# Kernel optimization log

Measured on AMD Instinct MI355X. Metric: run time of the kernel, lower is better.

## Reference

```python
import jax, jax.numpy as jnp
import numpy as np

DIM = 192
HEADS = 6
HSP = 8
WSP = 8
POS_DIM = (DIM // 4) // 4  # 12


def _ln(x, g, b, eps=1e-5):
    m = jnp.mean(x, -1, keepdims=True)
    v = jnp.mean((x - m) ** 2, -1, keepdims=True)
    return (x - m) / jnp.sqrt(v + eps) * g + b


def _rel_tables():
    # rpe_biases: ((2*HSP-1)*(2*WSP-1), 2) float coords of all relative offsets
    bh, bw = np.meshgrid(np.arange(1 - HSP, HSP), np.arange(1 - WSP, WSP), indexing='ij')
    biases = np.stack([bh, bw], -1).reshape(-1, 2).astype(np.float32)
    # relative_position_index: (N, N) int lookup into the bias table
    ch, cw = np.meshgrid(np.arange(HSP), np.arange(WSP), indexing='ij')
    coords = np.stack([ch, cw], 0).reshape(2, -1)  # (2, N)
    rel = coords[:, :, None] - coords[:, None, :]  # (2, N, N)
    idx = (rel[0] + HSP - 1) * (2 * WSP - 1) + (rel[1] + WSP - 1)
    return jnp.asarray(biases), jnp.asarray(idx.astype(np.int32))


def setup_inputs() -> dict:
    key = jax.random.key(0)
    ks = jax.random.split(key, 8)
    B, H, W = 2, 256, 256
    L = H * W
    def lin(k, i, o):
        return jax.random.normal(k, (i, o), jnp.float32) * 0.02
    return {
        'qkv': jax.random.normal(ks[0], (3, B, L, DIM), jnp.float32),
        'w_proj': lin(ks[1], 2, POS_DIM), 'b_proj': jnp.zeros((POS_DIM,), jnp.float32),
        'g1': jnp.ones((POS_DIM,), jnp.float32), 'be1': jnp.zeros((POS_DIM,), jnp.float32),
        'w1': lin(ks[2], POS_DIM, POS_DIM), 'b1': jnp.zeros((POS_DIM,), jnp.float32),
        'g2': jnp.ones((POS_DIM,), jnp.float32), 'be2': jnp.zeros((POS_DIM,), jnp.float32),
        'w2': lin(ks[3], POS_DIM, POS_DIM), 'b2': jnp.zeros((POS_DIM,), jnp.float32),
        'g3': jnp.ones((POS_DIM,), jnp.float32), 'be3': jnp.zeros((POS_DIM,), jnp.float32),
        'w3': lin(ks[4], POS_DIM, HEADS), 'b3': jnp.zeros((HEADS,), jnp.float32),
        'H': H, 'W': W,
    }


def reference(qkv, w_proj, b_proj, g1, be1, w1, b1, g2, be2, w2, b2, g3, be3, w3, b3, H, W):
    B, L, C = qkv.shape[1], qkv.shape[2], qkv.shape[3]
    hd = C // HEADS
    scale = float(hd) ** -0.5
    N = HSP * WSP

    def im2win(x):
        # (B, L, C) -> (B*nW, heads, N, hd)
        x = x.reshape(B, H // HSP, HSP, W // WSP, WSP, C)
        x = x.transpose(0, 1, 3, 2, 4, 5).reshape(-1, N, HEADS, hd)
        return x.transpose(0, 2, 1, 3)

    q = im2win(qkv[0]) * scale
    k = im2win(qkv[1])
    v = im2win(qkv[2])

    attn = jnp.einsum('whnd,whmd->whnm', q, k)  # (B*nW, heads, N, N)

    # dynamic relative position bias via MLP (DynamicPosBias, residual=False)
    biases, rel_idx = _rel_tables()
    p = biases @ w_proj + b_proj
    p = jax.nn.relu(_ln(p, g1, be1)) @ w1 + b1
    p = jax.nn.relu(_ln(p, g2, be2)) @ w2 + b2
    p = jax.nn.relu(_ln(p, g3, be3)) @ w3 + b3  # (n_rel, heads)
    rpb = p[rel_idx.reshape(-1)].reshape(N, N, HEADS).transpose(2, 0, 1)  # (heads, N, N)
    attn = attn + rpb[None]

    attn = jax.nn.softmax(attn, axis=-1)
    x = jnp.einsum('whnm,whmd->whnd', attn, v)  # (B*nW, heads, N, hd)
    x = x.transpose(0, 2, 1, 3).reshape(-1, N, C)

    # windows2img: (B*nW, N, C) -> (B, H, W, C)
    x = x.reshape(B, H // HSP, W // WSP, HSP, WSP, C)
    x = x.transpose(0, 1, 3, 2, 4, 5).reshape(B, H, W, C)
    return x
```

## Files before the change

### kernel.cpp

```cpp
#include <hip/hip_runtime.h>
#include <hip/hip_bf16.h>

#define NHEADS 6
#define HD 32
#define CDIM 192
#define NTOK 64
#define NREL 225
#define PDIM 12
#define IMG 256
#define NWIN 2048
#define SCALE 0.17677669529663687f
#define INV_SCALE 5.656854249492381f

typedef __attribute__((ext_vector_type(8))) short v8s;
typedef __attribute__((ext_vector_type(4))) float v4f;

#define KS2 200
#define VTS 72
#define PTS 72

__device__ __forceinline__ unsigned pkbf(float x, float y) {
    __hip_bfloat162 h = __float22bfloat162_rn(make_float2(x, y));
    union { __hip_bfloat162 h; unsigned u; } c; c.h = h;
    return c.u;
}

__device__ __forceinline__ void ln_relu12(const float* x, const float* g,
                                          const float* be, float* y) {
    float m = 0.f;
#pragma unroll
    for (int i = 0; i < PDIM; ++i) m += x[i];
    m *= (1.f / PDIM);
    float v = 0.f;
#pragma unroll
    for (int i = 0; i < PDIM; ++i) { float d = x[i] - m; v += d * d; }
    v *= (1.f / PDIM);
    float inv = rsqrtf(v + 1e-5f);
#pragma unroll
    for (int i = 0; i < PDIM; ++i) {
        float t = (x[i] - m) * inv * g[i] + be[i];
        y[i] = t > 0.f ? t : 0.f;
    }
}

__global__ __launch_bounds__(256) void win_attn_fused(
    const float* __restrict__ qkv,
    const float* __restrict__ wp, const float* __restrict__ bp,
    const float* __restrict__ g1, const float* __restrict__ be1,
    const float* __restrict__ w1, const float* __restrict__ b1,
    const float* __restrict__ g2, const float* __restrict__ be2,
    const float* __restrict__ w2, const float* __restrict__ b2,
    const float* __restrict__ g3, const float* __restrict__ be3,
    const float* __restrict__ w3, const float* __restrict__ b3,
    float* __restrict__ out)
{
    __shared__ __align__(16) unsigned short ks[NTOK * KS2];
    __shared__ __align__(16) unsigned short vt[CDIM * VTS];
    __shared__ __align__(16) unsigned short pt[NTOK * PTS];
    __shared__ float psh[NHEADS * NREL];

    const int t = threadIdx.x;
    const int win = blockIdx.x;
    const int b  = win >> 10;
    const int bh = (win >> 5) & 31;
    const int bw = win & 31;

    const int lane = t & 63;
    const int wave = t >> 6;
    const int lw = lane & 15;
    const int lg = lane >> 4;
    const int rowbase = wave * 16;

    const size_t PL = (size_t)2 * IMG * IMG * CDIM;
    const float* qplane = qkv + (size_t)b * IMG * IMG * CDIM;
    const float* kplane = qplane + PL;
    const float* vplane = kplane + PL;

    auto pixoff = [&](int tok) -> size_t {
        return ((size_t)(bh * 8 + (tok >> 3)) * IMG + (bw * 8 + (tok & 7))) * CDIM;
    };

#pragma unroll
    for (int pass = 0; pass < 12; ++pass) {
        int fidx = t + pass * 256;
        int s   = fidx / 384;
        int rem = fidx - s * 384;
        int j1  = rem / 48;
        int f   = rem - j1 * 48;
        float4 k4 = *(const float4*)(kplane
                     + ((size_t)(bh * 8 + s) * IMG + (bw * 8 + j1)) * CDIM + f * 4);
        uint2 kk; kk.x = pkbf(k4.x, k4.y); kk.y = pkbf(k4.z, k4.w);
        *(uint2*)&ks[(s * 8 + j1) * KS2 + f * 4] = kk;
    }

    {
        const int u  = t & 31;
        const int dg = t >> 5;
        const int ta = (u & 15) + (u >> 4) * 32;
        const int db = dg * 4;
        const int kpa = (u & 15) * 4 + (u >> 4) * 2;
        const size_t offa = pixoff(ta), offb = pixoff(ta + 16);
#pragma unroll
        for (int h = 0; h < NHEADS; ++h) {
            float4 va = *(const float4*)(vplane + offa + h * HD + db);
            float4 vb = *(const float4*)(vplane + offb + h * HD + db);
            int row = h * HD + db;
            *(unsigned*)&vt[(row + 0) * VTS + kpa] = pkbf(va.x, vb.x);
            *(unsigned*)&vt[(row + 1) * VTS + kpa] = pkbf(va.y, vb.y);
            *(unsigned*)&vt[(row + 2) * VTS + kpa] = pkbf(va.z, vb.z);
            *(unsigned*)&vt[(row + 3) * VTS + kpa] = pkbf(va.w, vb.w);
        }
    }

    v8s aq[NHEADS];
    {
        const size_t qoff = pixoff(rowbase + lw);
#pragma unroll
        for (int h = 0; h < NHEADS; ++h) {
            const float* qp = qplane + qoff + h * HD + lg * 8;
            float4 q0 = *(const float4*)qp;
            float4 q1 = *(const float4*)(qp + 4);
            union { v8s v; unsigned x[4]; } au;
            au.x[0] = pkbf(q0.x, q0.y);
            au.x[1] = pkbf(q0.z, q0.w);
            au.x[2] = pkbf(q1.x, q1.y);
            au.x[3] = pkbf(q1.z, q1.w);
            aq[h] = au.v;
        }
    }

    if (t < NREL) {
        float x0 = (float)(t / 15 - 7);
        float x1 = (float)(t % 15 - 7);
        float h[PDIM], y[PDIM];
#pragma unroll
        for (int o = 0; o < PDIM; ++o)
            h[o] = x0 * wp[o] + x1 * wp[PDIM + o] + bp[o];
        ln_relu12(h, g1, be1, y);
#pragma unroll
        for (int o = 0; o < PDIM; ++o) {
            float a = b1[o];
#pragma unroll
            for (int i = 0; i < PDIM; ++i) a += y[i] * w1[i * PDIM + o];
            h[o] = a;
        }
        ln_relu12(h, g2, be2, y);
#pragma unroll
        for (int o = 0; o < PDIM; ++o) {
            float a = b2[o];
#pragma unroll
            for (int i = 0; i < PDIM; ++i) a += y[i] * w2[i * PDIM + o];
            h[o] = a;
        }
        ln_relu12(h, g3, be3, y);
#pragma unroll
        for (int o = 0; o < NHEADS; ++o) {
            float a = b3[o];
#pragma unroll
            for (int i = 0; i < PDIM; ++i) a += y[i] * w3[i * NHEADS + o];
            psh[o * NREL + t] = a * INV_SCALE;
        }
    }
    __syncthreads();

    int base_r[4];
    size_t ooff[4];
#pragma unroll
    for (int r = 0; r < 4; ++r) {
        int n = rowbase + lg * 4 + r;
        base_r[r] = ((n >> 3) - (lw >> 3) + 7) * 15 + (n & 7) - (lw & 7) + 7;
        ooff[r] = ((size_t)(b * IMG + bh * 8 + (n >> 3)) * IMG
                   + (bw * 8 + (n & 7))) * CDIM;
    }

#pragma unroll
    for (int h = 0; h < NHEADS; ++h) {
        v4f acc[4];
#pragma unroll
        for (int ct = 0; ct < 4; ++ct) {
            v4f z = {0.f, 0.f, 0.f, 0.f};
            v8s bfr = *(const v8s*)&ks[(ct * 16 + lw) * KS2 + h * HD + lg * 8];
            acc[ct] = __builtin_amdgcn_mfma_f32_16x16x32_bf16(aq[h], bfr, z, 0, 0, 0);
        }
        const float* ph = &psh[h * NREL];
        v4f s4 = {0.f, 0.f, 0.f, 0.f};
#pragma unroll
        for (int ct = 0; ct < 4; ++ct)
#pragma unroll
            for (int r = 0; r < 4; ++r) {
                float e = __expf((acc[ct][r] + ph[base_r[r] - ct * 30]) * SCALE);
                acc[ct][r] = e;
                s4[r] += e;
            }
#pragma unroll
        for (int off = 1; off < 16; off <<= 1)
#pragma unroll
            for (int r = 0; r < 4; ++r)
                s4[r] += __shfl_xor(s4[r], off);
        v4f rinv;
#pragma unroll
        for (int r = 0; r < 4; ++r) rinv[r] = __builtin_amdgcn_rcpf(s4[r]);
#pragma unroll
        for (int r = 0; r < 4; ++r) {
            uint2 w;
            w.x = pkbf(acc[0][r], acc[1][r]);
            w.y = pkbf(acc[2][r], acc[3][r]);
            *(uint2*)&pt[(rowbase + lg * 4 + r) * PTS + lw * 4] = w;
        }
        v8s pa[2];
#pragma unroll
        for (int kt = 0; kt < 2; ++kt)
            pa[kt] = *(const v8s*)&pt[(rowbase + lw) * PTS + kt * 32 + lg * 8];
        v4f acc2[2] = {};
#pragma unroll
        for (int dt = 0; dt < 2; ++dt)
#pragma unroll
            for (int kt = 0; kt < 2; ++kt) {
                v8s vb = *(const v8s*)&vt[(h * HD + dt * 16 + lw) * VTS
                                          + kt * 32 + lg * 8];
                acc2[dt] = __builtin_amdgcn_mfma_f32_16x16x32_bf16(pa[kt], vb, acc2[dt], 0, 0, 0);
            }
#pragma unroll
        for (int dt = 0; dt < 2; ++dt)
#pragma unroll
            for (int r = 0; r < 4; ++r)
                out[ooff[r] + h * HD + dt * 16 + lw] = acc2[dt][r] * rinv[r];
    }
}

extern "C" void kernel_launch(void* const* d_in, const int* in_sizes, int n_in,
                              void* d_out, int out_size, void* d_ws, size_t ws_size,
                              hipStream_t stream) {
    const float* qkv = (const float*)d_in[0];
    win_attn_fused<<<NWIN, 256, 0, stream>>>(
        qkv,
        (const float*)d_in[1], (const float*)d_in[2],
        (const float*)d_in[3], (const float*)d_in[4],
        (const float*)d_in[5], (const float*)d_in[6],
        (const float*)d_in[7], (const float*)d_in[8],
        (const float*)d_in[9], (const float*)d_in[10],
        (const float*)d_in[11], (const float*)d_in[12],
        (const float*)d_in[13], (const float*)d_in[14],
        (float*)d_out);
}
```

Before: 92.45 us.

## Split heads across two wave groups with 512-thread blocks per window

Doubles the block to 512 threads, with waves 0-3 handling heads 0-2 and waves 4-7 handling heads 3-5 of each window. Loads are spread over twice as many threads, and the softmax probability staging buffer is duplicated per head group. This shortens each thread's serial work and adds wave-level parallelism, at the cost of more LDS per block and possibly fewer resident blocks per CU.

```diff
diff --git a/kernel.cpp b/kernel.cpp
--- a/kernel.cpp
+++ b/kernel.cpp
@@ -43,7 +43,7 @@
     }
 }
 
-__global__ __launch_bounds__(256) void win_attn_fused(
+__global__ __launch_bounds__(512) void win_attn_fused(
     const float* __restrict__ qkv,
     const float* __restrict__ wp, const float* __restrict__ bp,
     const float* __restrict__ g1, const float* __restrict__ be1,
@@ -56,7 +56,7 @@
 {
     __shared__ __align__(16) unsigned short ks[NTOK * KS2];
     __shared__ __align__(16) unsigned short vt[CDIM * VTS];
-    __shared__ __align__(16) unsigned short pt[NTOK * PTS];
+    __shared__ __align__(16) unsigned short pt[2][NTOK * PTS];
     __shared__ float psh[NHEADS * NREL];
 
     const int t = threadIdx.x;
@@ -67,9 +67,12 @@
 
     const int lane = t & 63;
     const int wave = t >> 6;
+    const int rg   = wave & 3;
+    const int hh   = wave >> 2;
+    const int hbase = hh * 3;
     const int lw = lane & 15;
     const int lg = lane >> 4;
-    const int rowbase = wave * 16;
+    const int rowbase = rg * 16;
 
     const size_t PL = (size_t)2 * IMG * IMG * CDIM;
     const float* qplane = qkv + (size_t)b * IMG * IMG * CDIM;
@@ -81,8 +84,8 @@
     };
 
 #pragma unroll
-    for (int pass = 0; pass < 12; ++pass) {
-        int fidx = t + pass * 256;
+    for (int pass = 0; pass < 6; ++pass) {
+        int fidx = t + pass * 512;
         int s   = fidx / 384;
         int rem = fidx - s * 384;
         int j1  = rem / 48;
@@ -95,13 +98,15 @@
 
     {
         const int u  = t & 31;
-        const int dg = t >> 5;
+        const int dg = (t >> 5) & 7;
+        const int vh = t >> 8;
         const int ta = (u & 15) + (u >> 4) * 32;
         const int db = dg * 4;
         const int kpa = (u & 15) * 4 + (u >> 4) * 2;
         const size_t offa = pixoff(ta), offb = pixoff(ta + 16);
 #pragma unroll
-        for (int h = 0; h < NHEADS; ++h) {
+        for (int hi = 0; hi < 3; ++hi) {
+            int h = vh * 3 + hi;
             float4 va = *(const float4*)(vplane + offa + h * HD + db);
             float4 vb = *(const float4*)(vplane + offb + h * HD + db);
             int row = h * HD + db;
@@ -112,12 +117,12 @@
         }
     }
 
-    v8s aq[NHEADS];
+    v8s aq[3];
     {
         const size_t qoff = pixoff(rowbase + lw);
 #pragma unroll
-        for (int h = 0; h < NHEADS; ++h) {
-            const float* qp = qplane + qoff + h * HD + lg * 8;
+        for (int hi = 0; hi < 3; ++hi) {
+            const float* qp = qplane + qoff + (hbase + hi) * HD + lg * 8;
             float4 q0 = *(const float4*)qp;
             float4 q1 = *(const float4*)(qp + 4);
             union { v8s v; unsigned x[4]; } au;
@@ -125,7 +130,7 @@
             au.x[1] = pkbf(q0.z, q0.w);
             au.x[2] = pkbf(q1.x, q1.y);
             au.x[3] = pkbf(q1.z, q1.w);
-            aq[h] = au.v;
+            aq[hi] = au.v;
         }
     }
 
@@ -174,13 +179,14 @@
     }
 
 #pragma unroll
-    for (int h = 0; h < NHEADS; ++h) {
+    for (int hi = 0; hi < 3; ++hi) {
+        const int h = hbase + hi;
         v4f acc[4];
 #pragma unroll
         for (int ct = 0; ct < 4; ++ct) {
             v4f z = {0.f, 0.f, 0.f, 0.f};
             v8s bfr = *(const v8s*)&ks[(ct * 16 + lw) * KS2 + h * HD + lg * 8];
-            acc[ct] = __builtin_amdgcn_mfma_f32_16x16x32_bf16(aq[h], bfr, z, 0, 0, 0);
+            acc[ct] = __builtin_amdgcn_mfma_f32_16x16x32_bf16(aq[hi], bfr, z, 0, 0, 0);
         }
         const float* ph = &psh[h * NREL];
         v4f s4 = {0.f, 0.f, 0.f, 0.f};
@@ -205,12 +211,12 @@
             uint2 w;
             w.x = pkbf(acc[0][r], acc[1][r]);
             w.y = pkbf(acc[2][r], acc[3][r]);
-            *(uint2*)&pt[(rowbase + lg * 4 + r) * PTS + lw * 4] = w;
+            *(uint2*)&pt[hh][(rowbase + lg * 4 + r) * PTS + lw * 4] = w;
         }
         v8s pa[2];
 #pragma unroll
         for (int kt = 0; kt < 2; ++kt)
-            pa[kt] = *(const v8s*)&pt[(rowbase + lw) * PTS + kt * 32 + lg * 8];
+            pa[kt] = *(const v8s*)&pt[hh][(rowbase + lw) * PTS + kt * 32 + lg * 8];
         v4f acc2[2] = {};
 #pragma unroll
         for (int dt = 0; dt < 2; ++dt)
@@ -232,7 +238,7 @@
                               void* d_out, int out_size, void* d_ws, size_t ws_size,
                               hipStream_t stream) {
     const float* qkv = (const float*)d_in[0];
-    win_attn_fused<<<NWIN, 256, 0, stream>>>(
+    win_attn_fused<<<NWIN, 512, 0, stream>>>(
         qkv,
         (const float*)d_in[1], (const float*)d_in[2],
         (const float*)d_in[3], (const float*)d_in[4],
```

Result: faster. 88.26 us (-4.5%).
